# Kernel optimization log

Hardware: AMD Instinct MI355X
Metric: run time of the kernel (lower is better)

## Reference

```python
import jax, jax.numpy as jnp
import numpy as np

DIM_HEAD = 64


def setup_inputs() -> dict:
    key = jax.random.key(0)
    ks = jax.random.split(key, 9)
    B, S, D, H, Dh = 1, 4096, 1024, 16, DIM_HEAD
    s = 0.02
    return {
        "x": jax.random.normal(ks[0], (B, S, D), jnp.float32),
        "wq": jax.random.normal(ks[1], (H, D, Dh), jnp.float32) * s,
        "bq": jax.random.normal(ks[2], (H, Dh), jnp.float32) * s,
        "wk": jax.random.normal(ks[3], (H, D, Dh), jnp.float32) * s,
        "bk": jax.random.normal(ks[4], (H, Dh), jnp.float32) * s,
        "wv": jax.random.normal(ks[5], (H, D, Dh), jnp.float32) * s,
        "bv": jax.random.normal(ks[6], (H, Dh), jnp.float32) * s,
        "wo": jax.random.normal(ks[7], (D, D), jnp.float32) * s,
        "bo": jax.random.normal(ks[8], (D,), jnp.float32) * s,
    }


def reference(x, wq, bq, wk, bk, wv, bv, wo, bo):
    # x: [B, S, D]; per-head projections batched over H (same math as
    # torch's per-head nn.Linear layers applied independently).
    B, S, D = x.shape
    H, _, Dh = wq.shape
    dot_scale = jnp.sqrt(jnp.asarray(Dh, x.dtype))
    q = jnp.einsum("bsd,hde->bhse", x, wq) + bq[None, :, None, :]  # [B,H,S,Dh]
    k = jnp.einsum("bsd,hde->bhse", x, wk) + bk[None, :, None, :]
    v = jnp.einsum("bsd,hde->bhse", x, wv) + bv[None, :, None, :]
    scores = jnp.einsum("bhse,bhte->bhst", q, k) / dot_scale        # [B,H,S,S]
    attn = jax.nn.softmax(scores, axis=-1)
    o = jnp.einsum("bhst,bhte->bhse", attn, v)                      # [B,H,S,Dh]
    # concat heads in head order -> [B, S, H*Dh]
    concat = jnp.transpose(o, (0, 2, 1, 3)).reshape(B, S, H * Dh)
    return concat @ wo + bo
```

## Files before the change

kernel.cpp:

```cpp
#include <hip/hip_runtime.h>
#include <hip/hip_bf16.h>

#define S_LEN 4096
#define DMODEL 1024
#define NHEAD 16
#define QKLD 2048

typedef __attribute__((ext_vector_type(8))) short s16x8;
typedef __attribute__((ext_vector_type(4))) float f32x4;

__device__ inline unsigned short f2bf(float f){
  unsigned u = __builtin_bit_cast(unsigned, f);
  u += 0x7FFFu + ((u >> 16) & 1u);
  return (unsigned short)(u >> 16);
}

__device__ inline float bf2f(unsigned short b){
  unsigned u = ((unsigned)b) << 16;
  return __builtin_bit_cast(float, u);
}

__device__ inline unsigned pk2bf(float a, float b){
  float2 t; t.x = a; t.y = b;
  __hip_bfloat162 h = __float22bfloat162_rn(t);
  unsigned r;
  __builtin_memcpy(&r, &h, 4);
  return r;
}

__device__ inline void gload_lds16(const void* g, void* l){
  __builtin_amdgcn_global_load_lds(
    (const __attribute__((address_space(1))) void*)g,
    (__attribute__((address_space(3))) void*)l, 16, 0, 0);
}

__global__ __launch_bounds__(256) void pack_all_kern(
    const float* __restrict__ x,
    const float* __restrict__ wq, const float* __restrict__ bq,
    const float* __restrict__ wk, const float* __restrict__ bk,
    const float* __restrict__ wv, const float* __restrict__ bv,
    const float* __restrict__ wo,
    unsigned short* __restrict__ xb, unsigned short* __restrict__ wt,
    float* __restrict__ bias, unsigned short* __restrict__ wot){
  int b = blockIdx.x, tid = threadIdx.x;
  if (b < 4096){
    int i = (b * 256 + tid) * 4;
    float4 v = *(const float4*)(x + i);
    ushort4 o;
    o.x = f2bf(v.x); o.y = f2bf(v.y); o.z = f2bf(v.z); o.w = f2bf(v.w);
    *(ushort4*)(xb + i) = o;
  } else if (b < 16384){
    int idx = (b - 4096) * 256 + tid;
    int which = idx >> 20;
    int rem = idx & 1048575;
    int e = rem & 63;
    int d = (rem >> 6) & 1023;
    int h = rem >> 16;
    const float* w = which == 0 ? wq : which == 1 ? wk : wv;
    const float* bb = which == 0 ? bq : which == 1 ? bk : bv;
    float scale = which == 0 ? 0.18033688011112042f : 1.0f;
    float val = w[(h * 1024 + d) * 64 + e] * scale;
    int n = which * 1024 + h * 64 + e;
    wt[(size_t)n * 1024 + d] = f2bf(val);
    if (d == 0) bias[n] = bb[h * 64 + e] * scale;
  } else {
    int idx = (b - 16384) * 256 + tid;
    int n = idx & 1023, d = idx >> 10;
    wot[(size_t)n * 1024 + d] = f2bf(wo[(size_t)d * 1024 + n]);
  }
}

__global__ __launch_bounds__(256) void gemm_qkv(const unsigned short* __restrict__ A,
                                                const unsigned short* __restrict__ Bt,
                                                const float* __restrict__ bias,
                                                unsigned short* __restrict__ Cout,
                                                unsigned short* __restrict__ vTout,
                                                int M, int N, int K){
  __shared__ unsigned short As[128 * 64];
  __shared__ unsigned short Bs[128 * 64];
  int tid = threadIdx.x;
  int lane = tid & 63, w = tid >> 6;
  int wr = w >> 1, wc = w & 1;
  int bid = blockIdx.x;
  int xcd = bid & 7, idx = bid >> 3;
  int mrow = (xcd << 2) + idx / 24;
  int ncol = idx % 24;
  int m0 = mrow * 128, n0 = ncol * 128;
  f32x4 zero = {0.f, 0.f, 0.f, 0.f};
  f32x4 acc[4][4];
#pragma unroll
  for (int i = 0; i < 4; i++)
#pragma unroll
    for (int j = 0; j < 4; j++) acc[i][j] = zero;

  for (int ks = 0; ks < K; ks += 64){
#pragma unroll
    for (int i = 0; i < 4; i++){
      int u = i * 256 + tid;
      int row = u >> 3, c = u & 7;
      gload_lds16(A + ((size_t)(m0 + row) * K + ks + ((c ^ (row & 7)) << 3)), &As[u * 8]);
    }
#pragma unroll
    for (int i = 0; i < 4; i++){
      int u = i * 256 + tid;
      int row = u >> 3, c = u & 7;
      gload_lds16(Bt + ((size_t)(n0 + row) * K + ks + ((c ^ (row & 7)) << 3)), &Bs[u * 8]);
    }
    __syncthreads();
#pragma unroll
    for (int kk = 0; kk < 2; kk++){
      s16x8 af[4], bfr[4];
#pragma unroll
      for (int i = 0; i < 4; i++){
        int ra = wr * 64 + i * 16 + (lane & 15);
        int ca = kk * 4 + (lane >> 4);
        af[i] = *(const s16x8*)&As[ra * 64 + ((ca ^ (ra & 7)) << 3)];
        int rb = wc * 64 + i * 16 + (lane & 15);
        bfr[i] = *(const s16x8*)&Bs[rb * 64 + ((ca ^ (rb & 7)) << 3)];
      }
#pragma unroll
      for (int i = 0; i < 4; i++)
#pragma unroll
        for (int j = 0; j < 4; j++)
          acc[i][j] = __builtin_amdgcn_mfma_f32_16x16x32_bf16(af[i], bfr[j], acc[i][j], 0, 0, 0);
    }
    __syncthreads();
  }
  int g = lane >> 4;
#pragma unroll
  for (int i = 0; i < 4; i++)
#pragma unroll
    for (int j = 0; j < 4; j++){
      int col = n0 + wc * 64 + j * 16 + (lane & 15);
      float bv = bias[col];
      if (n0 >= 2048){
        float v0 = acc[i][j][0] + bv, v1 = acc[i][j][1] + bv;
        float v2 = acc[i][j][2] + bv, v3 = acc[i][j][3] + bv;
        uint2 pkv; pkv.x = pk2bf(v0, v1); pkv.y = pk2bf(v2, v3);
        int p0 = 32 * (i >> 1) + 8 * g + 4 * (i & 1);
        *(uint2*)&vTout[(size_t)(col - 2048) * S_LEN + m0 + wr * 64 + p0] = pkv;
      } else {
#pragma unroll
        for (int r = 0; r < 4; r++){
          int row = m0 + wr * 64 + i * 16 + 4 * g + r;
          Cout[(size_t)row * QKLD + col] = f2bf(acc[i][j][r] + bv);
        }
      }
    }
}

__global__ __launch_bounds__(256) void gemm_bt_n64(const unsigned short* __restrict__ A,
                                                   const unsigned short* __restrict__ Bt,
                                                   const float* __restrict__ bias,
                                                   float* __restrict__ Cout,
                                                   int M, int N, int K){
  __shared__ unsigned short As[128 * 64];
  __shared__ unsigned short Bs[64 * 64];
  int tid = threadIdx.x;
  int lane = tid & 63, w = tid >> 6;
  int bid = blockIdx.x;
  int xcd = bid & 7, idx = bid >> 3;
  int mrow = (xcd << 2) + (idx >> 4);
  int ncol = idx & 15;
  int m0 = mrow * 128, n0 = ncol * 64;
  f32x4 zero = {0.f, 0.f, 0.f, 0.f};
  f32x4 acc[2][4];
#pragma unroll
  for (int i = 0; i < 2; i++)
#pragma unroll
    for (int j = 0; j < 4; j++) acc[i][j] = zero;

  for (int ks = 0; ks < K; ks += 64){
#pragma unroll
    for (int i = 0; i < 4; i++){
      int u = i * 256 + tid;
      int row = u >> 3, c = u & 7;
      gload_lds16(A + ((size_t)(m0 + row) * K + ks + ((c ^ (row & 7)) << 3)), &As[u * 8]);
    }
#pragma unroll
    for (int i = 0; i < 2; i++){
      int u = i * 256 + tid;
      int row = u >> 3, c = u & 7;
      gload_lds16(Bt + ((size_t)(n0 + row) * K + ks + ((c ^ (row & 7)) << 3)), &Bs[u * 8]);
    }
    __syncthreads();
#pragma unroll
    for (int kk = 0; kk < 2; kk++){
      s16x8 af[2], bfr[4];
#pragma unroll
      for (int i = 0; i < 2; i++){
        int ra = w * 32 + i * 16 + (lane & 15);
        int ca = kk * 4 + (lane >> 4);
        af[i] = *(const s16x8*)&As[ra * 64 + ((ca ^ (ra & 7)) << 3)];
      }
#pragma unroll
      for (int j = 0; j < 4; j++){
        int rb = j * 16 + (lane & 15);
        int ca = kk * 4 + (lane >> 4);
        bfr[j] = *(const s16x8*)&Bs[rb * 64 + ((ca ^ (rb & 7)) << 3)];
      }
#pragma unroll
      for (int i = 0; i < 2; i++)
#pragma unroll
        for (int j = 0; j < 4; j++)
          acc[i][j] = __builtin_amdgcn_mfma_f32_16x16x32_bf16(af[i], bfr[j], acc[i][j], 0, 0, 0);
    }
    __syncthreads();
  }
  int g = lane >> 4;
#pragma unroll
  for (int i = 0; i < 2; i++)
#pragma unroll
    for (int j = 0; j < 4; j++){
      int col = n0 + j * 16 + (lane & 15);
      float bv = bias[col];
#pragma unroll
      for (int r = 0; r < 4; r++){
        int row = m0 + w * 32 + i * 16 + 4 * g + r;
        Cout[(size_t)row * N + col] = acc[i][j][r] + bv;
      }
    }
}

template <bool SPLIT>
__global__ __launch_bounds__(512) void attn_kern(const unsigned short* __restrict__ qkv,
                                                 const unsigned short* __restrict__ vT,
                                                 unsigned short* __restrict__ concat,
                                                 unsigned short* __restrict__ numpart,
                                                 float* __restrict__ lpart){
  __shared__ unsigned short lds[16384];
  int tid = threadIdx.x, lane = tid & 63, w = tid >> 6;
  int q16 = lane & 15, g = lane >> 4;
  int bx, h, z;
  if (SPLIT){
    int lin = blockIdx.x;
    int xcd = lin & 7;
    int m = lin >> 3;
    int grp = xcd * 8 + (m >> 4);
    bx = m & 15;
    h = grp & 15;
    z = grp >> 4;
  } else {
    bx = blockIdx.x & 15;
    h = blockIdx.x >> 4;
    z = 0;
  }
  int ntiles = SPLIT ? (S_LEN / 256) : (S_LEN / 64);
  int kt0 = z * ntiles;
  int q0 = bx * 256 + w * 32;
  s16x8 qb[2][2];
#pragma unroll
  for (int qt = 0; qt < 2; qt++)
#pragma unroll
    for (int kk = 0; kk < 2; kk++)
      qb[qt][kk] = *(const s16x8*)&qkv[(size_t)(q0 + qt * 16 + q16) * QKLD + h * 64 + kk * 32 + g * 8];
  s16x8 ones;
#pragma unroll
  for (int j = 0; j < 8; j++) ones[j] = (short)0x3F80;
  f32x4 zero = {0.f, 0.f, 0.f, 0.f};
  f32x4 o[2][4];
  f32x4 l_acc[2];
#pragma unroll
  for (int qt = 0; qt < 2; qt++){
    l_acc[qt] = zero;
#pragma unroll
    for (int nc = 0; nc < 4; nc++) o[qt][nc] = zero;
  }
  int srow = tid >> 3, sc = tid & 7;
  int sswz = (sc ^ (srow & 7)) << 3;
  const unsigned short* kg0 = qkv + (size_t)(kt0 * 64 + srow) * QKLD + 1024 + h * 64 + sswz;
  const unsigned short* vg0 = vT + (size_t)(h * 64 + srow) * S_LEN + kt0 * 64 + sswz;
  int d0 = tid * 8;

#define STAGE(buf) do { \
    gload_lds16(kg0, &lds[(buf) * 4096 + d0]); \
    gload_lds16(vg0, &lds[8192 + (buf) * 4096 + d0]); \
    kg0 += 64 * QKLD; vg0 += 64; } while (0)

  STAGE(0);
  __syncthreads();
  int cur = 0;
  for (int it = 0; it < ntiles; it++){
    if (it + 1 < ntiles) STAGE(cur ^ 1);
    const unsigned short* Kc = &lds[cur * 4096];
    const unsigned short* Vc = &lds[8192 + cur * 4096];
    f32x4 s[2][4];
#pragma unroll
    for (int qt = 0; qt < 2; qt++)
#pragma unroll
      for (int ct = 0; ct < 4; ct++) s[qt][ct] = zero;
#pragma unroll
    for (int ct = 0; ct < 4; ct++)
#pragma unroll
      for (int kk = 0; kk < 2; kk++){
        int tr = ct * 16 + q16;
        int c = kk * 4 + g;
        s16x8 kf = *(const s16x8*)&Kc[tr * 64 + ((c ^ (tr & 7)) << 3)];
#pragma unroll
        for (int qt = 0; qt < 2; qt++)
          s[qt][ct] = __builtin_amdgcn_mfma_f32_16x16x32_bf16(kf, qb[qt][kk], s[qt][ct], 0, 0, 0);
      }
#pragma unroll
    for (int qt = 0; qt < 2; qt++)
#pragma unroll
      for (int ct = 0; ct < 4; ct++)
#pragma unroll
        for (int r = 0; r < 4; r++)
          s[qt][ct][r] = __builtin_amdgcn_exp2f(s[qt][ct][r]);
    s16x8 pb[2][2];
#pragma unroll
    for (int qt = 0; qt < 2; qt++)
#pragma unroll
      for (int kk = 0; kk < 2; kk++){
        union { unsigned u[4]; s16x8 v; } pk;
#pragma unroll
        for (int i = 0; i < 4; i++){
          int ct = 2 * kk + (i >> 1);
          int r = (i & 1) * 2;
          pk.u[i] = pk2bf(s[qt][ct][r], s[qt][ct][r + 1]);
        }
        pb[qt][kk] = pk.v;
      }
#pragma unroll
    for (int kk = 0; kk < 2; kk++)
#pragma unroll
      for (int qt = 0; qt < 2; qt++)
        l_acc[qt] = __builtin_amdgcn_mfma_f32_16x16x32_bf16(ones, pb[qt][kk], l_acc[qt], 0, 0, 0);
#pragma unroll
    for (int nc = 0; nc < 4; nc++)
#pragma unroll
      for (int kk = 0; kk < 2; kk++){
        int er = nc * 16 + q16;
        int c = kk * 4 + g;
        s16x8 vf = *(const s16x8*)&Vc[er * 64 + ((c ^ (er & 7)) << 3)];
#pragma unroll
        for (int qt = 0; qt < 2; qt++)
          o[qt][nc] = __builtin_amdgcn_mfma_f32_16x16x32_bf16(vf, pb[qt][kk], o[qt][nc], 0, 0, 0);
      }
    __syncthreads();
    cur ^= 1;
  }
#undef STAGE
#pragma unroll
  for (int qt = 0; qt < 2; qt++){
    size_t row = (size_t)(q0 + qt * 16 + q16);
    float l = l_acc[qt][0];
    if (SPLIT){
      if (g == 0) lpart[(size_t)z * (S_LEN * NHEAD) + row * NHEAD + h] = l;
#pragma unroll
      for (int nc = 0; nc < 4; nc++){
        uint2 pkv;
        pkv.x = pk2bf(o[qt][nc][0], o[qt][nc][1]);
        pkv.y = pk2bf(o[qt][nc][2], o[qt][nc][3]);
        *(uint2*)&numpart[(size_t)z * (S_LEN * DMODEL) + row * DMODEL + h * 64 + nc * 16 + 4 * g] = pkv;
      }
    } else {
      float inv = 1.0f / l;
#pragma unroll
      for (int nc = 0; nc < 4; nc++){
        uint2 pkv;
        pkv.x = pk2bf(o[qt][nc][0] * inv, o[qt][nc][1] * inv);
        pkv.y = pk2bf(o[qt][nc][2] * inv, o[qt][nc][3] * inv);
        *(uint2*)&concat[row * DMODEL + h * 64 + nc * 16 + 4 * g] = pkv;
      }
    }
  }
}

__global__ __launch_bounds__(256) void merge_kern(const unsigned short* __restrict__ numpart,
                                                  const float* __restrict__ lpart,
                                                  unsigned short* __restrict__ concat){
  int q = blockIdx.x, tid = threadIdx.x;
  int c = tid * 4;
  int h = c >> 6;
  float l = 0.f;
  float a0 = 0.f, a1 = 0.f, a2 = 0.f, a3 = 0.f;
#pragma unroll
  for (int z = 0; z < 4; z++){
    l += lpart[(size_t)z * (S_LEN * NHEAD) + q * NHEAD + h];
    ushort4 nv = *(const ushort4*)&numpart[(size_t)z * (S_LEN * DMODEL) + (size_t)q * DMODEL + c];
    a0 += bf2f(nv.x); a1 += bf2f(nv.y); a2 += bf2f(nv.z); a3 += bf2f(nv.w);
  }
  float inv = 1.0f / l;
  uint2 ov;
  ov.x = pk2bf(a0 * inv, a1 * inv);
  ov.y = pk2bf(a2 * inv, a3 * inv);
  *(uint2*)&concat[(size_t)q * DMODEL + c] = ov;
}

extern "C" void kernel_launch(void* const* d_in, const int* in_sizes, int n_in,
                              void* d_out, int out_size, void* d_ws, size_t ws_size,
                              hipStream_t stream){
  const float* x  = (const float*)d_in[0];
  const float* wq = (const float*)d_in[1];
  const float* bq = (const float*)d_in[2];
  const float* wk = (const float*)d_in[3];
  const float* bk = (const float*)d_in[4];
  const float* wv = (const float*)d_in[5];
  const float* bv = (const float*)d_in[6];
  const float* wo = (const float*)d_in[7];
  const float* bo = (const float*)d_in[8];
  char* ws = (char*)d_ws;
  unsigned short* xb      = (unsigned short*)(ws + 0);
  unsigned short* wqkvt   = (unsigned short*)(ws + 8388608);
  unsigned short* numpart = (unsigned short*)(ws + 0);
  unsigned short* wot     = (unsigned short*)(ws + 33554432);
  float*          biasq   = (float*)(ws + 35651584);
  unsigned short* qkv     = (unsigned short*)(ws + 35717120);
  unsigned short* vT      = (unsigned short*)(ws + 52494336);
  unsigned short* concat  = (unsigned short*)(ws + 60882944);
  float*          lpart   = (float*)(ws + 69271552);
  const size_t ws_need = 70320128;
  float* out = (float*)d_out;

  pack_all_kern<<<20480, 256, 0, stream>>>(x, wq, bq, wk, bk, wv, bv, wo,
                                           xb, wqkvt, biasq, wot);
  gemm_qkv<<<768, 256, 0, stream>>>(xb, wqkvt, biasq, qkv, vT, 4096, QKLD, 1024);
  if (ws_size >= ws_need){
    attn_kern<true><<<1024, 512, 0, stream>>>(qkv, vT, concat, numpart, lpart);
    merge_kern<<<4096, 256, 0, stream>>>(numpart, lpart, concat);
  } else {
    attn_kern<false><<<256, 512, 0, stream>>>(qkv, vT, concat, numpart, lpart);
  }
  gemm_bt_n64<<<512, 256, 0, stream>>>(concat, wot, bo, out, 4096, 1024, 1024);
}
```

Baseline: 160.5 us.

## Fuse split-KV merge into output projection GEMM and reorder QK MFMA loop

Replaces the separate merge kernel plus output GEMM with one kernel that sums the four split-KV partial numerators, normalizes by the summed denominators, and writes bf16 tiles straight into LDS as the A operand. This removes a kernel launch and the write and re-read of the concat buffer. In exchange, each of the 16 column blocks re-reads and re-merges the four partial numerator arrays, so merge traffic and ALU work are multiplied. The A loads are synchronous rather than async-to-LDS. The attention QK loop is also restructured to load both K fragments per column tile and to start from zero instead of a separate zeroing pass.

```diff
diff --git a/kernel.cpp b/kernel.cpp
--- a/kernel.cpp
+++ b/kernel.cpp
@@ -19,6 +19,9 @@
   unsigned u = ((unsigned)b) << 16;
   return __builtin_bit_cast(float, u);
 }
+
+__device__ inline float lo16f(unsigned d){ return __builtin_bit_cast(float, d << 16); }
+__device__ inline float hi16f(unsigned d){ return __builtin_bit_cast(float, d & 0xFFFF0000u); }
 
 __device__ inline unsigned pk2bf(float a, float b){
   float2 t; t.x = a; t.y = b;
@@ -149,6 +152,99 @@
     }
 }
 
+__global__ __launch_bounds__(256) void gemm_out_fused(const unsigned short* __restrict__ numpart,
+                                                      const float* __restrict__ lpart,
+                                                      const unsigned short* __restrict__ Bt,
+                                                      const float* __restrict__ bias,
+                                                      float* __restrict__ Cout){
+  __shared__ unsigned short As[128 * 64];
+  __shared__ unsigned short Bs[64 * 64];
+  const int ZS = 4194304;
+  const int LS = 65536;
+  int tid = threadIdx.x;
+  int lane = tid & 63, w = tid >> 6;
+  int bid = blockIdx.x;
+  int xcd = bid & 7, idx = bid >> 3;
+  int mrow = (xcd << 2) + (idx >> 4);
+  int ncol = idx & 15;
+  int m0 = mrow * 128, n0 = ncol * 64;
+  f32x4 zero = {0.f, 0.f, 0.f, 0.f};
+  f32x4 acc[2][4];
+#pragma unroll
+  for (int i = 0; i < 2; i++)
+#pragma unroll
+    for (int j = 0; j < 4; j++) acc[i][j] = zero;
+
+  for (int ks = 0; ks < 1024; ks += 64){
+    int h = ks >> 6;
+#pragma unroll
+    for (int i = 0; i < 2; i++){
+      int u = i * 256 + tid;
+      int row = u >> 3, c = u & 7;
+      gload_lds16(Bt + ((size_t)(n0 + row) * 1024 + ks + ((c ^ (row & 7)) << 3)), &Bs[u * 8]);
+    }
+#pragma unroll
+    for (int i = 0; i < 4; i++){
+      int u = i * 256 + tid;
+      int row = u >> 3, c = u & 7;
+      size_t base = (size_t)(m0 + row) * 1024 + ks + ((c ^ (row & 7)) << 3);
+      uint4 n0v = *(const uint4*)&numpart[base];
+      uint4 n1v = *(const uint4*)&numpart[ZS + base];
+      uint4 n2v = *(const uint4*)&numpart[2 * ZS + base];
+      uint4 n3v = *(const uint4*)&numpart[3 * ZS + base];
+      int lidx = (m0 + row) * NHEAD + h;
+      float l = lpart[lidx] + lpart[LS + lidx] + lpart[2 * LS + lidx] + lpart[3 * LS + lidx];
+      float inv = 1.0f / l;
+      union { unsigned u4[4]; s16x8 v; } st;
+      unsigned dw[4][4] = {{n0v.x, n1v.x, n2v.x, n3v.x}, {n0v.y, n1v.y, n2v.y, n3v.y},
+                           {n0v.z, n1v.z, n2v.z, n3v.z}, {n0v.w, n1v.w, n2v.w, n3v.w}};
+#pragma unroll
+      for (int d = 0; d < 4; d++){
+        float lo = (lo16f(dw[d][0]) + lo16f(dw[d][1])) + (lo16f(dw[d][2]) + lo16f(dw[d][3]));
+        float hi = (hi16f(dw[d][0]) + hi16f(dw[d][1])) + (hi16f(dw[d][2]) + hi16f(dw[d][3]));
+        st.u4[d] = pk2bf(lo * inv, hi * inv);
+      }
+      *(s16x8*)&As[u * 8] = st.v;
+    }
+    __syncthreads();
+#pragma unroll
+    for (int kk = 0; kk < 2; kk++){
+      s16x8 af[2], bfr[4];
+#pragma unroll
+      for (int i = 0; i < 2; i++){
+        int ra = w * 32 + i * 16 + (lane & 15);
+        int ca = kk * 4 + (lane >> 4);
+        af[i] = *(const s16x8*)&As[ra * 64 + ((ca ^ (ra & 7)) << 3)];
+      }
+#pragma unroll
+      for (int j = 0; j < 4; j++){
+        int rb = j * 16 + (lane & 15);
+        int ca = kk * 4 + (lane >> 4);
+        bfr[j] = *(const s16x8*)&Bs[rb * 64 + ((ca ^ (rb & 7)) << 3)];
+      }
+#pragma unroll
+      for (int i = 0; i < 2; i++)
+#pragma unroll
+        for (int j = 0; j < 4; j++)
+          acc[i][j] = __builtin_amdgcn_mfma_f32_16x16x32_bf16(af[i], bfr[j], acc[i][j], 0, 0, 0);
+    }
+    __syncthreads();
+  }
+  int g = lane >> 4;
+#pragma unroll
+  for (int i = 0; i < 2; i++)
+#pragma unroll
+    for (int j = 0; j < 4; j++){
+      int col = n0 + j * 16 + (lane & 15);
+      float bv = bias[col];
+#pragma unroll
+      for (int r = 0; r < 4; r++){
+        int row = m0 + w * 32 + i * 16 + 4 * g + r;
+        Cout[(size_t)row * 1024 + col] = acc[i][j][r] + bv;
+      }
+    }
+}
+
 __global__ __launch_bounds__(256) void gemm_bt_n64(const unsigned short* __restrict__ A,
                                                    const unsigned short* __restrict__ Bt,
                                                    const float* __restrict__ bias,
@@ -286,20 +382,16 @@
     const unsigned short* Vc = &lds[8192 + cur * 4096];
     f32x4 s[2][4];
 #pragma unroll
-    for (int qt = 0; qt < 2; qt++)
-#pragma unroll
-      for (int ct = 0; ct < 4; ct++) s[qt][ct] = zero;
-#pragma unroll
-    for (int ct = 0; ct < 4; ct++)
-#pragma unroll
-      for (int kk = 0; kk < 2; kk++){
-        int tr = ct * 16 + q16;
-        int c = kk * 4 + g;
-        s16x8 kf = *(const s16x8*)&Kc[tr * 64 + ((c ^ (tr & 7)) << 3)];
-#pragma unroll
-        for (int qt = 0; qt < 2; qt++)
-          s[qt][ct] = __builtin_amdgcn_mfma_f32_16x16x32_bf16(kf, qb[qt][kk], s[qt][ct], 0, 0, 0);
-      }
+    for (int ct = 0; ct < 4; ct++){
+      int tr = ct * 16 + q16;
+      s16x8 kf0 = *(const s16x8*)&Kc[tr * 64 + ((g ^ (tr & 7)) << 3)];
+      s16x8 kf1 = *(const s16x8*)&Kc[tr * 64 + (((4 + g) ^ (tr & 7)) << 3)];
+#pragma unroll
+      for (int qt = 0; qt < 2; qt++){
+        s[qt][ct] = __builtin_amdgcn_mfma_f32_16x16x32_bf16(kf0, qb[qt][0], zero, 0, 0, 0);
+        s[qt][ct] = __builtin_amdgcn_mfma_f32_16x16x32_bf16(kf1, qb[qt][1], s[qt][ct], 0, 0, 0);
+      }
+    }
 #pragma unroll
     for (int qt = 0; qt < 2; qt++)
 #pragma unroll
@@ -418,9 +510,9 @@
   gemm_qkv<<<768, 256, 0, stream>>>(xb, wqkvt, biasq, qkv, vT, 4096, QKLD, 1024);
   if (ws_size >= ws_need){
     attn_kern<true><<<1024, 512, 0, stream>>>(qkv, vT, concat, numpart, lpart);
-    merge_kern<<<4096, 256, 0, stream>>>(numpart, lpart, concat);
+    gemm_out_fused<<<512, 256, 0, stream>>>(numpart, lpart, wot, bo, out);
   } else {
     attn_kern<false><<<256, 512, 0, stream>>>(qkv, vT, concat, numpart, lpart);
-  }
-  gemm_bt_n64<<<512, 256, 0, stream>>>(concat, wot, bo, out, 4096, 1024, 1024);
-}
+    gemm_bt_n64<<<512, 256, 0, stream>>>(concat, wot, bo, out, 4096, 1024, 1024);
+  }
+}
```

New measurement: 218.9 us. +36.4%, slower.
